# Optimization experiments

Hardware: AMD Instinct MI355X
Metric: run time of the kernel (lower is better)

## Reference

```python
import jax, jax.numpy as jnp
import numpy as np

D = 1024
H = 8
K = 6
TEMP = 0.1
LN_EPS = 1e-5


def _ln(x, g, b):
    m = jnp.mean(x, axis=-1, keepdims=True)
    v = jnp.mean((x - m) ** 2, axis=-1, keepdims=True)
    return (x - m) / jnp.sqrt(v + LN_EPS) * g + b


def setup_inputs() -> dict:
    key = jax.random.key(0)
    ks = jax.random.split(key, 8)
    B, T = 8, 4096
    s = 0.02
    inp = {
        'video_features': jax.random.normal(ks[0], (B, T, D), jnp.float32),
        'query_embedding': jax.random.normal(ks[1], (B, D), jnp.float32),
        'mu_w1': jax.random.normal(ks[2], (D, D), jnp.float32) * s,
        'mu_b1': jnp.zeros((D,), jnp.float32),
        'mu_g': jnp.ones((D,), jnp.float32),
        'mu_be': jnp.zeros((D,), jnp.float32),
        'mu_w2': jax.random.normal(ks[3], (D, D), jnp.float32) * s,
        'mu_b2': jnp.zeros((D,), jnp.float32),
        'sg_w1': jax.random.normal(ks[4], (D, D), jnp.float32) * s,
        'sg_b1': jnp.zeros((D,), jnp.float32),
        'sg_g': jnp.ones((D,), jnp.float32),
        'sg_be': jnp.zeros((D,), jnp.float32),
        'sg_w2': jax.random.normal(ks[5], (D, D), jnp.float32) * s,
        'sg_b2': jnp.zeros((D,), jnp.float32),
        'in_w': jax.random.normal(ks[6], (3 * D, D), jnp.float32) * s,
        'in_b': jnp.zeros((3 * D,), jnp.float32),
        'out_w': jax.random.normal(ks[7], (D, D), jnp.float32) * s,
        'out_b': jnp.zeros((D,), jnp.float32),
    }
    return inp


def reference(video_features, query_embedding, mu_w1, mu_b1, mu_g, mu_be, mu_w2, mu_b2,
              sg_w1, sg_b1, sg_g, sg_be, sg_w2, sg_b2, in_w, in_b, out_w, out_b):
    B, T, _ = video_features.shape
    dh = D // H

    # mu / sigma estimators (Linear -> LN -> ReLU -> Linear [-> Softplus])
    mu_q = jax.nn.relu(_ln(query_embedding @ mu_w1.T + mu_b1, mu_g, mu_be)) @ mu_w2.T + mu_b2  # [B,D]
    sigma_q = jax.nn.softplus(
        jax.nn.relu(_ln(query_embedding @ sg_w1.T + sg_b1, sg_g, sg_be)) @ sg_w2.T + sg_b2) + 1e-6

    # Mahalanobis (diagonal) distances [B,T]
    centered = video_features - mu_q[:, None, :]
    dist = jnp.sum(centered ** 2 / sigma_q[:, None, :], axis=-1)

    # distance weights around the (torch lower) median
    med = jnp.sort(dist, axis=1)[:, (T - 1) // 2][:, None]
    dist_w = jnp.exp(-jnp.abs(dist - med) / TEMP)  # [B,T]

    # single-query multihead attention (torch MHA, averaged attn weights)
    wq, wk, wv = in_w[:D], in_w[D:2 * D], in_w[2 * D:]
    bq, bk, bv = in_b[:D], in_b[D:2 * D], in_b[2 * D:]
    q = (mu_q @ wq.T + bq).reshape(B, H, dh)                  # [B,H,dh]
    k = (video_features @ wk.T + bk).reshape(B, T, H, dh)     # [B,T,H,dh]
    scores = jnp.einsum('bhd,bthd->bht', q, k) / jnp.sqrt(jnp.asarray(dh, q.dtype))
    attn = jax.nn.softmax(scores, axis=-1)                    # [B,H,T]
    attn_w = jnp.mean(attn, axis=1)                           # [B,T] head-averaged

    combined = dist_w * attn_w  # [B,T]

    # greedy diverse top-k (farthest-point style), vectorized over batch
    ar = jnp.arange(T)
    idx0 = jnp.argmax(combined, axis=1)                       # [B]
    sel_mask = ar[None, :] == idx0[:, None]
    min_d = jnp.abs(ar[None, :] - idx0[:, None]).astype(combined.dtype)
    picks = [idx0]
    for _ in range(K - 1):
        score = jnp.where(sel_mask, -jnp.inf, min_d * combined)
        nxt = jnp.argmax(score, axis=1)
        picks.append(nxt)
        sel_mask = sel_mask | (ar[None, :] == nxt[:, None])
        min_d = jnp.minimum(min_d, jnp.abs(ar[None, :] - nxt[:, None]).astype(combined.dtype))
    indices = jnp.stack(picks, axis=1)  # [B,K]

    rep = jnp.take_along_axis(video_features, indices[:, :, None], axis=1)  # [B,K,D]

    # NTLBG loss
    rep_dist = jnp.take_along_axis(dist, indices, axis=1)  # [B,K]
    target = jnp.sort(rep_dist, axis=1)[:, (K - 1) // 2][:, None]
    ellipsoid = jnp.mean((rep_dist - target) ** 2)
    centered_rep = rep - mu_q[:, None, :]
    consistency = jnp.mean(jnp.sum(centered_rep ** 2 / sigma_q[:, None, :], axis=-1))
    sim = jnp.einsum('bkd,bjd->bkj', rep, rep)
    tri = jnp.triu(jnp.ones((K, K), rep.dtype), k=1)
    diversity = jnp.mean((sim * tri) ** 2)
    loss = ellipsoid + 0.1 * consistency + 0.05 * diversity

    return rep, indices, combined, dist, mu_q, sigma_q, loss
```

## Files before the change

### kernel.cpp

```cpp
#include <hip/hip_runtime.h>
#include <math.h>

#define BD   8
#define TT   4096
#define DD   1024
#define HH   8
#define KK   6
#define OFF_REP   0
#define OFF_IDX   49152
#define OFF_COMB  49200
#define OFF_DIST  81968
#define OFF_MU    114736
#define OFF_SG    122928
#define OFF_LOSS  131120
#define WS_X1     0
#define WS_H      16384
#define WS_Q      32768
#define WS_P      40960
#define WS_C      106496
#define WS_ISIG   106560
#define WS_SCORES 114752
#define WS_IDXI   376896

#define INV_SQRT_DH 0.08838834764831845f

__device__ __forceinline__ float softplus_f(float x) {
  return fmaxf(x, 0.0f) + log1pf(expf(-fabsf(x)));
}

__device__ __forceinline__ void gemv_rows_core(const float* __restrict__ in,
                                               const float* __restrict__ W,
                                               int row, float (*s_in)[DD], float acc[8]) {
  int tid = threadIdx.x;
  const float4* in4 = (const float4*)in;
  float4* s4 = (float4*)&s_in[0][0];
  for (int i = tid; i < 2048; i += 256) s4[i] = in4[i];
  __syncthreads();
  int lane = tid & 63;
  const float4* wr4 = (const float4*)(W + (size_t)row * DD);
#pragma unroll
  for (int b = 0; b < 8; ++b) acc[b] = 0.0f;
#pragma unroll
  for (int i = 0; i < 4; ++i) {
    int d4 = i * 64 + lane;
    float4 w4 = wr4[d4];
#pragma unroll
    for (int b = 0; b < 8; ++b) {
      float4 q4 = ((const float4*)&s_in[b][0])[d4];
      acc[b] += w4.x * q4.x + w4.y * q4.y + w4.z * q4.z + w4.w * q4.w;
    }
  }
#pragma unroll
  for (int off = 32; off; off >>= 1)
#pragma unroll
    for (int b = 0; b < 8; ++b) acc[b] += __shfl_xor(acc[b], off, 64);
}

__global__ __launch_bounds__(256) void k_gemv_pre(const float* __restrict__ qe,
    const float* __restrict__ W0, const float* __restrict__ W1,
    const float* __restrict__ b0, const float* __restrict__ b1, float* __restrict__ x1) {
  __shared__ float s_in[8][DD];
  int path = blockIdx.x >> 8;
  int row = (blockIdx.x & 255) * 4 + (threadIdx.x >> 6);
  const float* W = path ? W1 : W0;
  const float* bb = path ? b1 : b0;
  float acc[8];
  gemv_rows_core(qe, W, row, s_in, acc);
  if ((threadIdx.x & 63) == 0) {
    float bv = bb[row];
#pragma unroll
    for (int b = 0; b < 8; ++b) x1[path * 8192 + b * DD + row] = acc[b] + bv;
  }
}

__global__ __launch_bounds__(256) void k_ln(const float* __restrict__ x1,
    const float* __restrict__ g0, const float* __restrict__ be0,
    const float* __restrict__ g1, const float* __restrict__ be1, float* __restrict__ h) {
  int path = blockIdx.x >> 3, b = blockIdx.x & 7;
  const float* x = x1 + path * 8192 + b * DD;
  const float* g = path ? g1 : g0;
  const float* be = path ? be1 : be0;
  __shared__ float sx[DD];
  __shared__ float red[256];
  int tid = threadIdx.x;
  float ps = 0.0f;
  for (int i = tid; i < DD; i += 256) { float v = x[i]; sx[i] = v; ps += v; }
  red[tid] = ps; __syncthreads();
  for (int off = 128; off; off >>= 1) { if (tid < off) red[tid] += red[tid + off]; __syncthreads(); }
  float mean = red[0] * (1.0f / 1024.0f);
  __syncthreads();
  float pv = 0.0f;
  for (int i = tid; i < DD; i += 256) { float d = sx[i] - mean; pv += d * d; }
  red[tid] = pv; __syncthreads();
  for (int off = 128; off; off >>= 1) { if (tid < off) red[tid] += red[tid + off]; __syncthreads(); }
  float var = red[0] * (1.0f / 1024.0f);
  float inv = 1.0f / sqrtf(var + 1e-5f);
  for (int i = tid; i < DD; i += 256) {
    float v = (sx[i] - mean) * inv * g[i] + be[i];
    h[path * 8192 + b * DD + i] = v > 0.0f ? v : 0.0f;
  }
}

__global__ __launch_bounds__(256) void k_gemv_mid(const float* __restrict__ h,
    const float* __restrict__ W0, const float* __restrict__ W1,
    const float* __restrict__ b0, const float* __restrict__ b1,
    float* __restrict__ mu_out, float* __restrict__ sg_out, float* __restrict__ isig) {
  __shared__ float s_in[8][DD];
  int path = blockIdx.x >> 8;
  int row = (blockIdx.x & 255) * 4 + (threadIdx.x >> 6);
  const float* W = path ? W1 : W0;
  const float* bb = path ? b1 : b0;
  float acc[8];
  gemv_rows_core(h + path * 8192, W, row, s_in, acc);
  if ((threadIdx.x & 63) == 0) {
    float bv = bb[row];
#pragma unroll
    for (int b = 0; b < 8; ++b) {
      float v = acc[b] + bv;
      if (path == 0) {
        mu_out[b * DD + row] = v;
      } else {
        float sp = softplus_f(v) + 1e-6f;
        sg_out[b * DD + row] = sp;
        isig[b * DD + row] = 1.0f / sp;
      }
    }
  }
}

__global__ __launch_bounds__(256) void k_gemv_q(const float* __restrict__ mu_q,
    const float* __restrict__ in_w, const float* __restrict__ in_b, float* __restrict__ q) {
  __shared__ float s_in[8][DD];
  int row = blockIdx.x * 4 + (threadIdx.x >> 6);
  float acc[8];
  gemv_rows_core(mu_q, in_w, row, s_in, acc);
  if ((threadIdx.x & 63) == 0) {
    float bv = in_b[row];
#pragma unroll
    for (int b = 0; b < 8; ++b) q[b * DD + row] = acc[b] + bv;
  }
}

__global__ __launch_bounds__(256) void k_p(const float* __restrict__ q,
    const float* __restrict__ in_w, const float* __restrict__ in_b,
    float* __restrict__ p, float* __restrict__ c) {
  int hh = blockIdx.x >> 2;
  int j0 = (blockIdx.x & 3) * 256;
  __shared__ float qh[8][128];
  for (int i = threadIdx.x; i < 1024; i += 256) {
    int b = i >> 7, r = i & 127;
    qh[b][r] = q[b * DD + hh * 128 + r];
  }
  __syncthreads();
  const float* wbase = in_w + (size_t)(DD + hh * 128) * DD + j0 + threadIdx.x;
  float acc[8];
#pragma unroll
  for (int b = 0; b < 8; ++b) acc[b] = 0.0f;
  for (int r = 0; r < 128; ++r) {
    float w = wbase[(size_t)r * DD];
#pragma unroll
    for (int b = 0; b < 8; ++b) acc[b] += qh[b][r] * w;
  }
#pragma unroll
  for (int b = 0; b < 8; ++b) p[(b * HH + hh) * DD + j0 + threadIdx.x] = acc[b] * INV_SQRT_DH;
  if ((blockIdx.x & 3) == 0 && threadIdx.x < 8) {
    int b = threadIdx.x;
    float cc = 0.0f;
    for (int r = 0; r < 128; ++r) cc += qh[b][r] * in_b[DD + hh * 128 + r];
    c[b * HH + hh] = cc * INV_SQRT_DH;
  }
}

__global__ __launch_bounds__(256, 4) void k_main(const float* __restrict__ video,
    const float* __restrict__ mu_q, const float* __restrict__ isig,
    const float* __restrict__ p, const float* __restrict__ c,
    float* __restrict__ dist_out, float* __restrict__ scores) {
  __shared__ float s_mu[DD];
  __shared__ float s_is[DD];
  __shared__ float s_p[HH][DD];
  int b = blockIdx.x >> 8;
  int chunk = blockIdx.x & 255;
  int tid = threadIdx.x;
  int wave = tid >> 6, lane = tid & 63;
  float4* s_mu4 = (float4*)s_mu;
  float4* s_is4 = (float4*)s_is;
  float4* s_p4 = (float4*)&s_p[0][0];
  s_mu4[tid] = ((const float4*)(mu_q + b * DD))[tid];
  s_is4[tid] = ((const float4*)(isig + b * DD))[tid];
  const float4* pg4 = (const float4*)(p + b * HH * DD);
  for (int i = tid; i < 2048; i += 256) s_p4[i] = pg4[i];
  __syncthreads();

  int t0 = chunk * 16 + wave * 4;
  const float4* v4 = (const float4*)(video + ((size_t)(b * TT + t0)) * DD);
  double dacc[4] = {0.0, 0.0, 0.0, 0.0};
  float sacc[4][8];
#pragma unroll
  for (int t = 0; t < 4; ++t)
#pragma unroll
    for (int hh = 0; hh < 8; ++hh) sacc[t][hh] = 0.0f;

#pragma unroll 2
  for (int i = 0; i < 4; ++i) {
    int d4 = i * 64 + lane;
    float4 vv0 = v4[0 * 256 + d4];
    float4 vv1 = v4[1 * 256 + d4];
    float4 vv2 = v4[2 * 256 + d4];
    float4 vv3 = v4[3 * 256 + d4];
    {
      float4 mu4 = s_mu4[d4];
      float4 is4 = s_is4[d4];
      float dx, dy, dz, dw, e;
      dx = vv0.x - mu4.x; dy = vv0.y - mu4.y; dz = vv0.z - mu4.z; dw = vv0.w - mu4.w;
      e = dx * dx * is4.x + dy * dy * is4.y + dz * dz * is4.z + dw * dw * is4.w;
      dacc[0] += (double)e;
      dx = vv1.x - mu4.x; dy = vv1.y - mu4.y; dz = vv1.z - mu4.z; dw = vv1.w - mu4.w;
      e = dx * dx * is4.x + dy * dy * is4.y + dz * dz * is4.z + dw * dw * is4.w;
      dacc[1] += (double)e;
      dx = vv2.x - mu4.x; dy = vv2.y - mu4.y; dz = vv2.z - mu4.z; dw = vv2.w - mu4.w;
      e = dx * dx * is4.x + dy * dy * is4.y + dz * dz * is4.z + dw * dw * is4.w;
      dacc[2] += (double)e;
      dx = vv3.x - mu4.x; dy = vv3.y - mu4.y; dz = vv3.z - mu4.z; dw = vv3.w - mu4.w;
      e = dx * dx * is4.x + dy * dy * is4.y + dz * dz * is4.z + dw * dw * is4.w;
      dacc[3] += (double)e;
    }
#pragma unroll
    for (int hh = 0; hh < 8; ++hh) {
      float4 pp = ((const float4*)&s_p[hh][0])[d4];
      sacc[0][hh] += pp.x * vv0.x + pp.y * vv0.y + pp.z * vv0.z + pp.w * vv0.w;
      sacc[1][hh] += pp.x * vv1.x + pp.y * vv1.y + pp.z * vv1.z + pp.w * vv1.w;
      sacc[2][hh] += pp.x * vv2.x + pp.y * vv2.y + pp.z * vv2.z + pp.w * vv2.w;
      sacc[3][hh] += pp.x * vv3.x + pp.y * vv3.y + pp.z * vv3.z + pp.w * vv3.w;
    }
  }
#pragma unroll
  for (int off = 32; off; off >>= 1) {
#pragma unroll
    for (int t = 0; t < 4; ++t) {
      dacc[t] += __shfl_xor(dacc[t], off, 64);
#pragma unroll
      for (int hh = 0; hh < 8; ++hh) sacc[t][hh] += __shfl_xor(sacc[t][hh], off, 64);
    }
  }
  if (lane < 4) {
    int t = lane;
    int tt = t0 + t;
    dist_out[b * TT + tt] = (float)dacc[t];
#pragma unroll
    for (int hh = 0; hh < 8; ++hh)
      scores[(size_t)(b * HH + hh) * TT + tt] = sacc[t][hh] + c[b * HH + hh];
  }
}

__global__ __launch_bounds__(256) void k_softmax(float* __restrict__ scores) {
  float* s = scores + (size_t)blockIdx.x * TT;
  __shared__ float buf[TT];
  __shared__ float red[256];
  int tid = threadIdx.x;
  float m = -INFINITY;
  for (int i = tid; i < TT; i += 256) { float v = s[i]; buf[i] = v; m = fmaxf(m, v); }
  red[tid] = m; __syncthreads();
  for (int off = 128; off; off >>= 1) { if (tid < off) red[tid] = fmaxf(red[tid], red[tid + off]); __syncthreads(); }
  float mx = red[0];
  __syncthreads();
  float ps = 0.0f;
  for (int i = tid; i < TT; i += 256) { float e = expf(buf[i] - mx); buf[i] = e; ps += e; }
  red[tid] = ps; __syncthreads();
  for (int off = 128; off; off >>= 1) { if (tid < off) red[tid] += red[tid + off]; __syncthreads(); }
  float inv = 1.0f / red[0];
  for (int i = tid; i < TT; i += 256) s[i] = buf[i] * inv;
}

__global__ __launch_bounds__(1024) void k_median(const float* __restrict__ dist,
    const float* __restrict__ attn, float* __restrict__ combined) {
  int b = blockIdx.x;
  __shared__ float s[TT];
  for (int i = threadIdx.x; i < TT; i += 1024) s[i] = dist[b * TT + i];
  __syncthreads();
  for (int k = 2; k <= TT; k <<= 1) {
    for (int j = k >> 1; j > 0; j >>= 1) {
      for (int i = threadIdx.x; i < TT; i += 1024) {
        int ixj = i ^ j;
        if (ixj > i) {
          float a = s[i], c2 = s[ixj];
          bool up = ((i & k) == 0);
          if ((a > c2) == up) { s[i] = c2; s[ixj] = a; }
        }
      }
      __syncthreads();
    }
  }
  float med = s[(TT - 1) / 2];
  for (int i = threadIdx.x; i < TT; i += 1024) {
    float d = dist[b * TT + i];
    float dw = expf(-fabsf(d - med) / 0.1f);
    float aw = 0.0f;
#pragma unroll
    for (int hh = 0; hh < HH; ++hh) aw += attn[(size_t)(b * HH + hh) * TT + i];
    combined[b * TT + i] = dw * (aw * 0.125f);
  }
}

__global__ __launch_bounds__(256) void k_select(const float* __restrict__ combined,
    float* __restrict__ idx_out, int* __restrict__ idx_ws, float* __restrict__ loss_out) {
  int b = blockIdx.x;
  int tid = threadIdx.x;
  int wave = tid >> 6, lane = tid & 63;
  if (b == 0 && tid == 0) loss_out[0] = 0.0f;
  __shared__ float comb[TT];
  __shared__ float mind[TT];
  __shared__ float wv[4];
  __shared__ int wi[4];
  __shared__ int s_pick;
  for (int i = tid; i < TT; i += 256) comb[i] = combined[b * TT + i];
  __syncthreads();
  int picks[KK];
  for (int k = 0; k < KK; ++k) {
    float best = -INFINITY; int bi = 1 << 30;
    for (int i = tid; i < TT; i += 256) {
      float cv = comb[i];
      float sc = (k == 0) ? cv : ((cv < 0.0f) ? -INFINITY : mind[i] * cv);
      if (sc > best) { best = sc; bi = i; }
    }
#pragma unroll
    for (int off = 32; off; off >>= 1) {
      float ov = __shfl_xor(best, off, 64);
      int oi = __shfl_xor(bi, off, 64);
      if (ov > best || (ov == best && oi < bi)) { best = ov; bi = oi; }
    }
    if (lane == 0) { wv[wave] = best; wi[wave] = bi; }
    __syncthreads();
    if (tid == 0) {
      float bb2 = wv[0]; int ii = wi[0];
#pragma unroll
      for (int w = 1; w < 4; ++w)
        if (wv[w] > bb2 || (wv[w] == bb2 && wi[w] < ii)) { bb2 = wv[w]; ii = wi[w]; }
      s_pick = ii;
      comb[ii] = -1.0f;
    }
    __syncthreads();
    int pick = s_pick;
    picks[k] = pick;
    for (int i = tid; i < TT; i += 256) {
      float dnew = fabsf((float)(i - pick));
      mind[i] = (k == 0) ? dnew : fminf(mind[i], dnew);
    }
  }
  if (tid < KK) {
    idx_out[b * KK + tid] = (float)picks[tid];
    idx_ws[b * KK + tid] = picks[tid];
  }
}

__global__ __launch_bounds__(256) void k_final(const float* __restrict__ video,
    const float* __restrict__ dist, const int* __restrict__ idx,
    float* __restrict__ rep, float* __restrict__ loss_out) {
  int b = blockIdx.x;
  __shared__ float repb[KK * DD];
  __shared__ float wdiv[4];
  __shared__ float s_rd[KK];
  int tid = threadIdx.x;
  int wave = tid >> 6, lane = tid & 63;
  const int pk[15] = {0,0,0,0,0,1,1,1,1,2,2,2,3,3,4};
  const int pj[15] = {1,2,3,4,5,2,3,4,5,3,4,5,4,5,5};
  float4* repb4 = (float4*)repb;
  float4* rep4 = (float4*)(rep + (size_t)b * KK * DD);
  for (int e = tid; e < KK * (DD / 4); e += 256) {
    int k = e >> 8, d4 = e & 255;
    const float4* vrow = (const float4*)(video + ((size_t)(b * TT + idx[b * KK + k])) * DD);
    float4 v = vrow[d4];
    rep4[(size_t)k * (DD / 4) + d4] = v;
    repb4[k * (DD / 4) + d4] = v;
  }
  if (tid < KK) s_rd[tid] = dist[b * TT + idx[b * KK + tid]];
  __syncthreads();
  float divacc = 0.0f;
  for (int pid = wave; pid < 15; pid += 4) {
    int kk = pk[pid], jj = pj[pid];
    float part = 0.0f;
    for (int d = lane; d < DD; d += 64) part += repb[kk * DD + d] * repb[jj * DD + d];
#pragma unroll
    for (int off = 32; off; off >>= 1) part += __shfl_xor(part, off, 64);
    if (lane == 0) divacc += part * part;
  }
  if (lane == 0) wdiv[wave] = divacc;
  __syncthreads();
  if (tid == 0) {
    float div = wdiv[0] + wdiv[1] + wdiv[2] + wdiv[3];
    float rd[KK], srt[KK];
#pragma unroll
    for (int k = 0; k < KK; ++k) { rd[k] = s_rd[k]; srt[k] = rd[k]; }
    for (int a = 1; a < KK; ++a) {
      float key = srt[a]; int b2 = a - 1;
      while (b2 >= 0 && srt[b2] > key) { srt[b2 + 1] = srt[b2]; --b2; }
      srt[b2 + 1] = key;
    }
    float target = srt[(KK - 1) / 2];
    float ell = 0.0f, cons = 0.0f;
#pragma unroll
    for (int k = 0; k < KK; ++k) { float d = rd[k] - target; ell += d * d; cons += rd[k]; }
    float partial = ell * (1.0f / 48.0f) + 0.1f * cons * (1.0f / 48.0f) + 0.05f * div * (1.0f / 288.0f);
    atomicAdd(loss_out, partial);
  }
}

extern "C" void kernel_launch(void* const* d_in, const int* in_sizes, int n_in,
                              void* d_out, int out_size, void* d_ws, size_t ws_size,
                              hipStream_t stream) {
  const float* video = (const float*)d_in[0];
  const float* qe    = (const float*)d_in[1];
  const float* mu_w1 = (const float*)d_in[2];
  const float* mu_b1 = (const float*)d_in[3];
  const float* mu_g  = (const float*)d_in[4];
  const float* mu_be = (const float*)d_in[5];
  const float* mu_w2 = (const float*)d_in[6];
  const float* mu_b2 = (const float*)d_in[7];
  const float* sg_w1 = (const float*)d_in[8];
  const float* sg_b1 = (const float*)d_in[9];
  const float* sg_g  = (const float*)d_in[10];
  const float* sg_be = (const float*)d_in[11];
  const float* sg_w2 = (const float*)d_in[12];
  const float* sg_b2 = (const float*)d_in[13];
  const float* in_w  = (const float*)d_in[14];
  const float* in_b  = (const float*)d_in[15];
  float* out = (float*)d_out;
  float* ws  = (float*)d_ws;
  int* idx_ws = (int*)(ws + WS_IDXI);

  k_gemv_pre<<<512, 256, 0, stream>>>(qe, mu_w1, sg_w1, mu_b1, sg_b1, ws + WS_X1);
  k_ln<<<16, 256, 0, stream>>>(ws + WS_X1, mu_g, mu_be, sg_g, sg_be, ws + WS_H);
  k_gemv_mid<<<512, 256, 0, stream>>>(ws + WS_H, mu_w2, sg_w2, mu_b2, sg_b2,
                                      out + OFF_MU, out + OFF_SG, ws + WS_ISIG);
  k_gemv_q<<<256, 256, 0, stream>>>(out + OFF_MU, in_w, in_b, ws + WS_Q);
  k_p<<<32, 256, 0, stream>>>(ws + WS_Q, in_w, in_b, ws + WS_P, ws + WS_C);
  k_main<<<2048, 256, 0, stream>>>(video, out + OFF_MU, ws + WS_ISIG, ws + WS_P, ws + WS_C,
                                   out + OFF_DIST, ws + WS_SCORES);
  k_softmax<<<64, 256, 0, stream>>>(ws + WS_SCORES);
  k_median<<<8, 1024, 0, stream>>>(out + OFF_DIST, ws + WS_SCORES, out + OFF_COMB);
  k_select<<<8, 256, 0, stream>>>(out + OFF_COMB, out + OFF_IDX, idx_ws, out + OFF_LOSS);
  k_final<<<8, 256, 0, stream>>>(video, out + OFF_DIST, idx_ws, out + OFF_REP, out + OFF_LOSS);
}
```

Measured before the change: 390.6 us.

## Fuse softmax, median, selection and loss into one epilogue kernel with radix-select median

Replaces four tail kernels (softmax, bitonic-sort median, greedy selection, final loss) with a single per-batch epilogue kernel. The median is found with a 4-pass 8-bit radix select over the float bits instead of a full bitonic sort. Softmax statistics are computed per head and applied on the fly, so the normalized scores are never written back. Loss zeroing moves into k_main. This removes launch overhead and a slow serial sort, but the work now runs on only 8 blocks, and the radix select relies on all distances being non-negative.

Result: faster. 380.7 us (-2.5%).

```diff
diff --git a/kernel.cpp b/kernel.cpp
--- a/kernel.cpp
+++ b/kernel.cpp
@@ -20,7 +20,6 @@
 #define WS_C      106496
 #define WS_ISIG   106560
 #define WS_SCORES 114752
-#define WS_IDXI   376896
 
 #define INV_SQRT_DH 0.08838834764831845f
 
@@ -174,7 +173,7 @@
 __global__ __launch_bounds__(256, 4) void k_main(const float* __restrict__ video,
     const float* __restrict__ mu_q, const float* __restrict__ isig,
     const float* __restrict__ p, const float* __restrict__ c,
-    float* __restrict__ dist_out, float* __restrict__ scores) {
+    float* __restrict__ dist_out, float* __restrict__ scores, float* __restrict__ loss_out) {
   __shared__ float s_mu[DD];
   __shared__ float s_is[DD];
   __shared__ float s_p[HH][DD];
@@ -182,6 +181,7 @@
   int chunk = blockIdx.x & 255;
   int tid = threadIdx.x;
   int wave = tid >> 6, lane = tid & 63;
+  if (blockIdx.x == 0 && tid == 0) loss_out[0] = 0.0f;
   float4* s_mu4 = (float4*)s_mu;
   float4* s_is4 = (float4*)s_is;
   float4* s_p4 = (float4*)&s_p[0][0];
@@ -252,74 +252,96 @@
   }
 }
 
-__global__ __launch_bounds__(256) void k_softmax(float* __restrict__ scores) {
-  float* s = scores + (size_t)blockIdx.x * TT;
-  __shared__ float buf[TT];
-  __shared__ float red[256];
-  int tid = threadIdx.x;
-  float m = -INFINITY;
-  for (int i = tid; i < TT; i += 256) { float v = s[i]; buf[i] = v; m = fmaxf(m, v); }
-  red[tid] = m; __syncthreads();
-  for (int off = 128; off; off >>= 1) { if (tid < off) red[tid] = fmaxf(red[tid], red[tid + off]); __syncthreads(); }
-  float mx = red[0];
-  __syncthreads();
-  float ps = 0.0f;
-  for (int i = tid; i < TT; i += 256) { float e = expf(buf[i] - mx); buf[i] = e; ps += e; }
-  red[tid] = ps; __syncthreads();
-  for (int off = 128; off; off >>= 1) { if (tid < off) red[tid] += red[tid + off]; __syncthreads(); }
-  float inv = 1.0f / red[0];
-  for (int i = tid; i < TT; i += 256) s[i] = buf[i] * inv;
-}
-
-__global__ __launch_bounds__(1024) void k_median(const float* __restrict__ dist,
-    const float* __restrict__ attn, float* __restrict__ combined) {
-  int b = blockIdx.x;
-  __shared__ float s[TT];
-  for (int i = threadIdx.x; i < TT; i += 1024) s[i] = dist[b * TT + i];
-  __syncthreads();
-  for (int k = 2; k <= TT; k <<= 1) {
-    for (int j = k >> 1; j > 0; j >>= 1) {
-      for (int i = threadIdx.x; i < TT; i += 1024) {
-        int ixj = i ^ j;
-        if (ixj > i) {
-          float a = s[i], c2 = s[ixj];
-          bool up = ((i & k) == 0);
-          if ((a > c2) == up) { s[i] = c2; s[ixj] = a; }
-        }
-      }
-      __syncthreads();
-    }
-  }
-  float med = s[(TT - 1) / 2];
-  for (int i = threadIdx.x; i < TT; i += 1024) {
-    float d = dist[b * TT + i];
-    float dw = expf(-fabsf(d - med) / 0.1f);
-    float aw = 0.0f;
-#pragma unroll
-    for (int hh = 0; hh < HH; ++hh) aw += attn[(size_t)(b * HH + hh) * TT + i];
-    combined[b * TT + i] = dw * (aw * 0.125f);
-  }
-}
-
-__global__ __launch_bounds__(256) void k_select(const float* __restrict__ combined,
-    float* __restrict__ idx_out, int* __restrict__ idx_ws, float* __restrict__ loss_out) {
+__global__ __launch_bounds__(256) void k_epilogue(const float* __restrict__ scores,
+    const float* __restrict__ dist, const float* __restrict__ video,
+    float* __restrict__ comb_out, float* __restrict__ idx_out,
+    float* __restrict__ rep, float* __restrict__ loss_out) {
   int b = blockIdx.x;
   int tid = threadIdx.x;
   int wave = tid >> 6, lane = tid & 63;
-  if (b == 0 && tid == 0) loss_out[0] = 0.0f;
-  __shared__ float comb[TT];
-  __shared__ float mind[TT];
+  __shared__ float s_aw[TT];
+  __shared__ float s_comb[TT];
+  __shared__ float s_mind[TT];
+  __shared__ float s_dist[TT];
+  __shared__ float s_hm[HH], s_hs[HH];
+  __shared__ unsigned hist[256];
+  __shared__ unsigned wsum[4];
+  __shared__ unsigned s_sel;
+  __shared__ int s_kk;
   __shared__ float wv[4];
   __shared__ int wi[4];
   __shared__ int s_pick;
-  for (int i = tid; i < TT; i += 256) comb[i] = combined[b * TT + i];
-  __syncthreads();
+  __shared__ float wdiv[4];
+
+  {
+    int h = tid >> 5, lt = tid & 31;
+    const float* srow = scores + ((size_t)(b * HH + h)) * TT;
+    float m = -INFINITY;
+    for (int i = lt; i < TT; i += 32) m = fmaxf(m, srow[i]);
+#pragma unroll
+    for (int off = 16; off; off >>= 1) m = fmaxf(m, __shfl_xor(m, off, 64));
+    float s = 0.0f;
+    for (int i = lt; i < TT; i += 32) s += expf(srow[i] - m);
+#pragma unroll
+    for (int off = 16; off; off >>= 1) s += __shfl_xor(s, off, 64);
+    if (lt == 0) { s_hm[h] = m; s_hs[h] = 1.0f / s; }
+  }
+  __syncthreads();
+  for (int i = tid; i < TT; i += 256) {
+    float aw = 0.0f;
+#pragma unroll
+    for (int h = 0; h < HH; ++h)
+      aw += expf(scores[((size_t)(b * HH + h)) * TT + i] - s_hm[h]) * s_hs[h];
+    s_aw[i] = aw * 0.125f;
+    s_dist[i] = dist[b * TT + i];
+  }
+  __syncthreads();
+
+  unsigned prefix = 0;
+  int kk = (TT - 1) / 2;
+  for (int pass = 0; pass < 4; ++pass) {
+    int shift = 24 - 8 * pass;
+    hist[tid] = 0;
+    __syncthreads();
+    for (int i = tid; i < TT; i += 256) {
+      unsigned key = __float_as_uint(s_dist[i]);
+      bool ok = (pass == 0) || ((key >> (shift + 8)) == prefix);
+      if (ok) atomicAdd(&hist[(key >> shift) & 255], 1u);
+    }
+    __syncthreads();
+    unsigned h = hist[tid];
+    unsigned inc = h;
+#pragma unroll
+    for (int off = 1; off < 64; off <<= 1) {
+      unsigned v = __shfl_up(inc, off, 64);
+      if (lane >= off) inc += v;
+    }
+    if (lane == 63) wsum[wave] = inc;
+    __syncthreads();
+    unsigned base = 0;
+    for (int w = 0; w < wave; ++w) base += wsum[w];
+    unsigned excl = base + inc - h;
+    if ((int)excl <= kk && kk < (int)(excl + h)) { s_sel = (prefix << 8) | (unsigned)tid; s_kk = kk - (int)excl; }
+    __syncthreads();
+    prefix = s_sel;
+    kk = s_kk;
+    __syncthreads();
+  }
+  float med = __uint_as_float(prefix);
+
+  for (int i = tid; i < TT; i += 256) {
+    float cv = expf(-fabsf(s_dist[i] - med) / 0.1f) * s_aw[i];
+    s_comb[i] = cv;
+    comb_out[b * TT + i] = cv;
+  }
+  __syncthreads();
+
   int picks[KK];
   for (int k = 0; k < KK; ++k) {
     float best = -INFINITY; int bi = 1 << 30;
     for (int i = tid; i < TT; i += 256) {
-      float cv = comb[i];
-      float sc = (k == 0) ? cv : ((cv < 0.0f) ? -INFINITY : mind[i] * cv);
+      float cv = s_comb[i];
+      float sc = (k == 0) ? cv : ((cv < 0.0f) ? -INFINITY : s_mind[i] * cv);
       if (sc > best) { best = sc; bi = i; }
     }
 #pragma unroll
@@ -336,49 +358,37 @@
       for (int w = 1; w < 4; ++w)
         if (wv[w] > bb2 || (wv[w] == bb2 && wi[w] < ii)) { bb2 = wv[w]; ii = wi[w]; }
       s_pick = ii;
-      comb[ii] = -1.0f;
+      s_comb[ii] = -1.0f;
     }
     __syncthreads();
     int pick = s_pick;
     picks[k] = pick;
     for (int i = tid; i < TT; i += 256) {
       float dnew = fabsf((float)(i - pick));
-      mind[i] = (k == 0) ? dnew : fminf(mind[i], dnew);
-    }
-  }
-  if (tid < KK) {
-    idx_out[b * KK + tid] = (float)picks[tid];
-    idx_ws[b * KK + tid] = picks[tid];
-  }
-}
-
-__global__ __launch_bounds__(256) void k_final(const float* __restrict__ video,
-    const float* __restrict__ dist, const int* __restrict__ idx,
-    float* __restrict__ rep, float* __restrict__ loss_out) {
-  int b = blockIdx.x;
+      s_mind[i] = (k == 0) ? dnew : fminf(s_mind[i], dnew);
+    }
+  }
+  if (tid < KK) idx_out[b * KK + tid] = (float)picks[tid];
+
   __shared__ float repb[KK * DD];
-  __shared__ float wdiv[4];
-  __shared__ float s_rd[KK];
-  int tid = threadIdx.x;
-  int wave = tid >> 6, lane = tid & 63;
-  const int pk[15] = {0,0,0,0,0,1,1,1,1,2,2,2,3,3,4};
-  const int pj[15] = {1,2,3,4,5,2,3,4,5,3,4,5,4,5,5};
   float4* repb4 = (float4*)repb;
   float4* rep4 = (float4*)(rep + (size_t)b * KK * DD);
   for (int e = tid; e < KK * (DD / 4); e += 256) {
     int k = e >> 8, d4 = e & 255;
-    const float4* vrow = (const float4*)(video + ((size_t)(b * TT + idx[b * KK + k])) * DD);
+    const float4* vrow = (const float4*)(video + ((size_t)(b * TT + picks[0])) * DD);
+    vrow = (const float4*)(video + ((size_t)(b * TT + picks[e >> 8])) * DD);
     float4 v = vrow[d4];
     rep4[(size_t)k * (DD / 4) + d4] = v;
     repb4[k * (DD / 4) + d4] = v;
   }
-  if (tid < KK) s_rd[tid] = dist[b * TT + idx[b * KK + tid]];
-  __syncthreads();
+  __syncthreads();
+  const int pk[15] = {0,0,0,0,0,1,1,1,1,2,2,2,3,3,4};
+  const int pj[15] = {1,2,3,4,5,2,3,4,5,3,4,5,4,5,5};
   float divacc = 0.0f;
   for (int pid = wave; pid < 15; pid += 4) {
-    int kk = pk[pid], jj = pj[pid];
+    int a = pk[pid], j = pj[pid];
     float part = 0.0f;
-    for (int d = lane; d < DD; d += 64) part += repb[kk * DD + d] * repb[jj * DD + d];
+    for (int d = lane; d < DD; d += 64) part += repb[a * DD + d] * repb[j * DD + d];
 #pragma unroll
     for (int off = 32; off; off >>= 1) part += __shfl_xor(part, off, 64);
     if (lane == 0) divacc += part * part;
@@ -389,7 +399,7 @@
     float div = wdiv[0] + wdiv[1] + wdiv[2] + wdiv[3];
     float rd[KK], srt[KK];
 #pragma unroll
-    for (int k = 0; k < KK; ++k) { rd[k] = s_rd[k]; srt[k] = rd[k]; }
+    for (int k = 0; k < KK; ++k) { rd[k] = s_dist[picks[k]]; srt[k] = rd[k]; }
     for (int a = 1; a < KK; ++a) {
       float key = srt[a]; int b2 = a - 1;
       while (b2 >= 0 && srt[b2] > key) { srt[b2 + 1] = srt[b2]; --b2; }
@@ -425,7 +435,6 @@
   const float* in_b  = (const float*)d_in[15];
   float* out = (float*)d_out;
   float* ws  = (float*)d_ws;
-  int* idx_ws = (int*)(ws + WS_IDXI);
 
   k_gemv_pre<<<512, 256, 0, stream>>>(qe, mu_w1, sg_w1, mu_b1, sg_b1, ws + WS_X1);
   k_ln<<<16, 256, 0, stream>>>(ws + WS_X1, mu_g, mu_be, sg_g, sg_be, ws + WS_H);
@@ -434,9 +443,7 @@
   k_gemv_q<<<256, 256, 0, stream>>>(out + OFF_MU, in_w, in_b, ws + WS_Q);
   k_p<<<32, 256, 0, stream>>>(ws + WS_Q, in_w, in_b, ws + WS_P, ws + WS_C);
   k_main<<<2048, 256, 0, stream>>>(video, out + OFF_MU, ws + WS_ISIG, ws + WS_P, ws + WS_C,
-                                   out + OFF_DIST, ws + WS_SCORES);
-  k_softmax<<<64, 256, 0, stream>>>(ws + WS_SCORES);
-  k_median<<<8, 1024, 0, stream>>>(out + OFF_DIST, ws + WS_SCORES, out + OFF_COMB);
-  k_select<<<8, 256, 0, stream>>>(out + OFF_COMB, out + OFF_IDX, idx_ws, out + OFF_LOSS);
-  k_final<<<8, 256, 0, stream>>>(video, out + OFF_DIST, idx_ws, out + OFF_REP, out + OFF_LOSS);
-}
+                                   out + OFF_DIST, ws + WS_SCORES, out + OFF_LOSS);
+  k_epilogue<<<8, 256, 0, stream>>>(ws + WS_SCORES, out + OFF_DIST, video,
+                                    out + OFF_COMB, out + OFF_IDX, out + OFF_REP, out + OFF_LOSS);
+}
```
